# Kernel tuning notes

Hardware: AMD Instinct MI355X
Metric: run time of the kernel (lower is better)

Reference implementation:

```python
import jax, jax.numpy as jnp
import numpy as np

N = 500          # max_neurons, all alive
INPUT_SIZE = 3072
FEAT_DIM = 64
OUT_SIZE = 10
BATCH = 8192
RADIUS = 20.0
VOL = 100.0      # cubic volume (100,100,100)
N_ITER = 3


def setup_inputs() -> dict:
    key = jax.random.key(0)
    k_x, k_pos, k_iw, k_f, k_ow = jax.random.split(key, 5)
    x = jax.random.normal(k_x, (BATCH, INPUT_SIZE), dtype=jnp.float32)
    # seed positions spread across the volume, roughly matching _init_seeds
    positions = jax.random.uniform(k_pos, (N, 3), dtype=jnp.float32) * 80.0 + 10.0
    input_weights = jax.random.normal(k_iw, (N, INPUT_SIZE), dtype=jnp.float32) * 0.02
    features = jax.random.normal(k_f, (N, FEAT_DIM), dtype=jnp.float32) * 0.1
    output_weights = jax.random.normal(k_ow, (N, OUT_SIZE), dtype=jnp.float32) * 0.02
    biases = jnp.zeros((N,), dtype=jnp.float32)
    return {"x": x, "positions": positions, "input_weights": input_weights,
            "features": features, "output_weights": output_weights, "biases": biases}


def reference(x, positions, input_weights, features, output_weights, biases):
    # clamp positions into the volume (per-axis, vol is cubic here)
    pos = jnp.clip(positions, 0.1, VOL - 0.1)  # [N,3]

    # pairwise distances (grad-safe sqrt at the zero diagonal)
    diff = pos[:, None, :] - pos[None, :, :]          # [N,N,3]
    sq = jnp.sum(diff * diff, axis=-1)                # [N,N]
    pos_mask = sq > 0.0
    dist = jnp.where(pos_mask, jnp.sqrt(jnp.where(pos_mask, sq, 1.0)), 0.0)

    conn_mask = (dist < RADIUS) & (dist > 0.0)
    attenuation = jnp.exp(-dist / RADIUS) * conn_mask.astype(dist.dtype)

    # feature similarity (F.normalize clamps the norm from below at eps)
    feat_norm = features / jnp.maximum(
        jnp.linalg.norm(features, axis=1, keepdims=True), 1e-6)
    feat_sim = jnp.clip(feat_norm @ feat_norm.T, -1.0, 1.0)  # [N,N]

    conn_w = attenuation * (0.5 + 0.5 * feat_sim)
    conn_w = conn_w / (jnp.sum(conn_w, axis=1, keepdims=True) + 1e-6)

    # input gating: neurons near x=0 receive input
    x_norm = pos[:, 0] / VOL                          # [N]
    input_weight = jnp.exp(-2.0 * x_norm)
    input_weight = input_weight / (jnp.sum(input_weight) + 1e-6)

    activations = x @ input_weights.T * input_weight + biases  # [B,N]

    # iterative message passing (fixed small iteration count)
    for _ in range(N_ITER):
        msg = activations @ conn_w.T                  # [B,N]
        activations = jnp.minimum(jax.nn.relu(activations + 0.5 * msg), 50.0)

    # output gating: neurons near x=VOL emit output
    output_weight = jnp.exp(2.0 * (x_norm - 1.0))
    output_weight = output_weight / (jnp.sum(output_weight) + 1e-6)

    return activations @ (output_weights * output_weight[:, None])  # [B,OUT]
```

## Files before the change

### kernel.cpp

```cpp
#include <hip/hip_runtime.h>
#include <stdint.h>

#define N_REAL 500
#define NPAD   512
#define K_IN   3072
#define NBATCH 8192
#define NOUT   10
#define RADIUS 20.0f
#define VOLF   100.0f

typedef __attribute__((ext_vector_type(8))) __bf16 bf16x8;
typedef __attribute__((ext_vector_type(4))) float  f32x4;
typedef __attribute__((ext_vector_type(4))) unsigned short us4;

__device__ __forceinline__ unsigned short f2bf(float f) {
    unsigned int u = __float_as_uint(f);
    u += 0x7FFFu + ((u >> 16) & 1u);
    return (unsigned short)(u >> 16);
}
__device__ __forceinline__ float bf2f(unsigned short h) {
    return __uint_as_float(((unsigned int)h) << 16);
}

#define GLOBAL_AS __attribute__((address_space(1)))
#define LDS_AS    __attribute__((address_space(3)))
__device__ __forceinline__ void glds16(const void* g, void* l) {
    __builtin_amdgcn_global_load_lds((const GLOBAL_AS void*)g, (LDS_AS void*)l, 16, 0, 0);
}

__global__ void prep1(const float* __restrict__ positions,
                      const float* __restrict__ features,
                      const float* __restrict__ out_w,
                      const float* __restrict__ biases,
                      float* __restrict__ feat_norm,
                      float* __restrict__ pos_c,
                      float* __restrict__ inw,
                      float* __restrict__ biasp,
                      float* __restrict__ wout)
{
    int n = threadIdx.x;
    float e_in = 0.f, e_out = 0.f;
    float px = 0.f, py = 0.f, pz = 0.f;
    if (n < N_REAL) {
        px = fminf(fmaxf(positions[n*3+0], 0.1f), VOLF - 0.1f);
        py = fminf(fmaxf(positions[n*3+1], 0.1f), VOLF - 0.1f);
        pz = fminf(fmaxf(positions[n*3+2], 0.1f), VOLF - 0.1f);
        float xn = px / VOLF;
        e_in  = expf(-2.f * xn);
        e_out = expf(2.f * (xn - 1.f));
        float ss = 0.f;
        for (int f = 0; f < 64; ++f) { float v = features[n*64+f]; ss += v*v; }
        float nm = fmaxf(sqrtf(ss), 1e-6f);
        for (int f = 0; f < 64; ++f) feat_norm[n*64+f] = features[n*64+f] / nm;
    } else {
        for (int f = 0; f < 64; ++f) feat_norm[n*64+f] = 0.f;
    }
    pos_c[n*4+0] = px; pos_c[n*4+1] = py; pos_c[n*4+2] = pz; pos_c[n*4+3] = 0.f;

    __shared__ float s_in[512], s_out[512];
    s_in[n] = e_in; s_out[n] = e_out;
    __syncthreads();
    for (int s = 256; s > 0; s >>= 1) {
        if (n < s) { s_in[n] += s_in[n+s]; s_out[n] += s_out[n+s]; }
        __syncthreads();
    }
    float sum_in  = s_in[0]  + 1e-6f;
    float sum_out = s_out[0] + 1e-6f;

    inw[n]   = (n < N_REAL) ? (e_in / sum_in) : 0.f;
    biasp[n] = (n < N_REAL) ? biases[n] : 0.f;
    float wo = (n < N_REAL) ? (e_out / sum_out) : 0.f;
    for (int o = 0; o < NOUT; ++o)
        wout[n*NOUT + o] = (n < N_REAL) ? out_w[n*NOUT + o] * wo : 0.f;
}

__global__ void prep2(const float* __restrict__ pos_c,
                      const float* __restrict__ feat_norm,
                      unsigned short* __restrict__ conn_w)
{
    int i = blockIdx.x;
    int t = threadIdx.x;
    __shared__ float fi[64];
    __shared__ float spos[4];
    __shared__ float red[128];
    if (t < 64) fi[t] = feat_norm[i*64 + t];
    if (t < 4)  spos[t] = pos_c[i*4 + t];
    __syncthreads();

    float w[4];
    float part = 0.f;
    for (int jj = 0; jj < 4; ++jj) {
        int j = t + jj*128;
        float val = 0.f;
        if (i < N_REAL && j < N_REAL) {
            float dx = spos[0] - pos_c[j*4+0];
            float dy = spos[1] - pos_c[j*4+1];
            float dz = spos[2] - pos_c[j*4+2];
            float sq = dx*dx + dy*dy + dz*dz;
            if (sq > 0.f) {
                float dist = sqrtf(sq);
                if (dist < RADIUS) {
                    float att = expf(-dist / RADIUS);
                    float sim = 0.f;
                    const float4* fj = (const float4*)(feat_norm + j*64);
                    const float4* fi4 = (const float4*)fi;
                    #pragma unroll
                    for (int f = 0; f < 16; ++f) {
                        float4 a = fi4[f]; float4 b = fj[f];
                        sim += a.x*b.x + a.y*b.y + a.z*b.z + a.w*b.w;
                    }
                    sim = fminf(fmaxf(sim, -1.f), 1.f);
                    val = att * (0.5f + 0.5f*sim);
                }
            }
        }
        w[jj] = val; part += val;
    }
    red[t] = part;
    __syncthreads();
    for (int s = 64; s > 0; s >>= 1) {
        if (t < s) red[t] += red[t+s];
        __syncthreads();
    }
    float inv = 1.f / (red[0] + 1e-6f);
    for (int jj = 0; jj < 4; ++jj)
        conn_w[(long)i*NPAD + t + jj*128] = f2bf(w[jj] * inv);
}

__global__ void cast_pad(const float* __restrict__ src, unsigned short* __restrict__ dst,
                         long total_q, long src_q)
{
    long i = (long)blockIdx.x * blockDim.x + threadIdx.x;
    long stride = (long)gridDim.x * blockDim.x;
    for (; i < total_q; i += stride) {
        us4 o;
        if (i < src_q) {
            float4 v = ((const float4*)src)[i];
            o[0] = f2bf(v.x); o[1] = f2bf(v.y); o[2] = f2bf(v.z); o[3] = f2bf(v.w);
        } else {
            o[0] = 0; o[1] = 0; o[2] = 0; o[3] = 0;
        }
        ((us4*)dst)[i] = o;
    }
}

__device__ __forceinline__ void block_map(int b, int& m0, int& n0) {
    int xcd = b & 7, loc = b >> 3;
    m0 = (xcd*8 + (loc >> 3)) * 128;
    n0 = (loc & 7) * 64;
}

__global__ __launch_bounds__(256)
void gemm1(const float* __restrict__ X,
           const unsigned short* __restrict__ B,
           unsigned short* __restrict__ Cbf,
           const float* __restrict__ inw,
           const float* __restrict__ biasp)
{
    __shared__ unsigned short As[128*64];
    __shared__ unsigned short Bs[64*64];

    const int tid  = threadIdx.x;
    const int lane = tid & 63;
    const int wave = tid >> 6;
    int m0, n0; block_map(blockIdx.x, m0, n0);
    const int wm = (wave >> 1) * 64;
    const int wn = (wave & 1) * 32;

    f32x4 acc[4][2];
    #pragma unroll
    for (int i = 0; i < 4; ++i)
        #pragma unroll
        for (int j = 0; j < 2; ++j)
            acc[i][j] = (f32x4){0.f,0.f,0.f,0.f};

    const float4* gA[8]; unsigned short* lA[8];
    #pragma unroll
    for (int s = 0; s < 8; ++s) {
        int f = tid + s*256;
        int row = f >> 4, c4 = f & 15;
        gA[s] = (const float4*)(X + (long)(m0 + row) * K_IN) + c4;
        lA[s] = (unsigned short*)((char*)As + row*128 + ((c4*8) ^ ((row & 7) << 4)));
    }
    const char* gB[2]; char* lB[2];
    #pragma unroll
    for (int s = 0; s < 2; ++s) {
        int o = tid*16 + s*4096;
        int row = o >> 7, d = o & 127;
        gB[s] = (const char*)B + (long)(n0 + row) * (K_IN*2) + (d ^ ((row & 7) << 4));
        lB[s] = (char*)Bs + o;
    }

    for (int k0 = 0; k0 < K_IN; k0 += 64) {
        __syncthreads();
        glds16(gB[0], lB[0]);
        glds16(gB[1], lB[1]);
        gB[0] += 128; gB[1] += 128;
        float4 v[8];
        #pragma unroll
        for (int s = 0; s < 8; ++s) v[s] = gA[s][0];
        #pragma unroll
        for (int s = 0; s < 8; ++s) {
            us4 o;
            o[0] = f2bf(v[s].x); o[1] = f2bf(v[s].y);
            o[2] = f2bf(v[s].z); o[3] = f2bf(v[s].w);
            *(us4*)lA[s] = o;
            gA[s] += 16;
        }
        asm volatile("s_waitcnt vmcnt(0) lgkmcnt(0)" ::: "memory");
        __syncthreads();

        #pragma unroll
        for (int kk = 0; kk < 2; ++kk) {
            const int cb = kk*64 + (lane >> 4) * 16;
            bf16x8 af[4], bfv[2];
            #pragma unroll
            for (int i = 0; i < 4; ++i) {
                int r = wm + i*16 + (lane & 15);
                af[i] = *(const bf16x8*)((const char*)As + r*128 + (cb ^ ((r & 7) << 4)));
            }
            #pragma unroll
            for (int j = 0; j < 2; ++j) {
                int r = wn + j*16 + (lane & 15);
                bfv[j] = *(const bf16x8*)((const char*)Bs + r*128 + (cb ^ ((r & 7) << 4)));
            }
            #pragma unroll
            for (int i = 0; i < 4; ++i)
                #pragma unroll
                for (int j = 0; j < 2; ++j)
                    acc[i][j] = __builtin_amdgcn_mfma_f32_16x16x32_bf16(af[i], bfv[j], acc[i][j], 0, 0, 0);
        }
    }

    const int mbase = m0 + wm + (lane >> 4) * 4;
    const int nbase = n0 + wn + (lane & 15);
    #pragma unroll
    for (int j = 0; j < 2; ++j) {
        const int n = nbase + j*16;
        const float win = inw[n], bia = biasp[n];
        #pragma unroll
        for (int i = 0; i < 4; ++i)
            #pragma unroll
            for (int r = 0; r < 4; ++r) {
                const long m = mbase + i*16 + r;
                Cbf[m*NPAD + n] = f2bf(acc[i][j][r] * win + bia);
            }
    }
}

__global__ __launch_bounds__(256)
void gemm2(const unsigned short* __restrict__ A,
           const unsigned short* __restrict__ B,
           unsigned short* __restrict__ Cbf,
           const unsigned short* __restrict__ actOld)
{
    __shared__ unsigned short As[128*64];
    __shared__ unsigned short Bs[64*64];

    const int tid  = threadIdx.x;
    const int lane = tid & 63;
    const int wave = tid >> 6;
    int m0, n0; block_map(blockIdx.x, m0, n0);
    const int wm = (wave >> 1) * 64;
    const int wn = (wave & 1) * 32;

    f32x4 acc[4][2];
    #pragma unroll
    for (int i = 0; i < 4; ++i)
        #pragma unroll
        for (int j = 0; j < 2; ++j)
            acc[i][j] = (f32x4){0.f,0.f,0.f,0.f};

    const char* gA[4]; char* lA[4];
    #pragma unroll
    for (int s = 0; s < 4; ++s) {
        int o = tid*16 + s*4096;
        int row = o >> 7, d = o & 127;
        gA[s] = (const char*)A + (long)(m0 + row) * (NPAD*2) + (d ^ ((row & 7) << 4));
        lA[s] = (char*)As + o;
    }
    const char* gB[2]; char* lB[2];
    #pragma unroll
    for (int s = 0; s < 2; ++s) {
        int o = tid*16 + s*4096;
        int row = o >> 7, d = o & 127;
        gB[s] = (const char*)B + (long)(n0 + row) * (NPAD*2) + (d ^ ((row & 7) << 4));
        lB[s] = (char*)Bs + o;
    }

    for (int k0 = 0; k0 < NPAD; k0 += 64) {
        __syncthreads();
        #pragma unroll
        for (int s = 0; s < 4; ++s) { glds16(gA[s], lA[s]); gA[s] += 128; }
        #pragma unroll
        for (int s = 0; s < 2; ++s) { glds16(gB[s], lB[s]); gB[s] += 128; }
        asm volatile("s_waitcnt vmcnt(0)" ::: "memory");
        __syncthreads();

        #pragma unroll
        for (int kk = 0; kk < 2; ++kk) {
            const int cb = kk*64 + (lane >> 4) * 16;
            bf16x8 af[4], bfv[2];
            #pragma unroll
            for (int i = 0; i < 4; ++i) {
                int r = wm + i*16 + (lane & 15);
                af[i] = *(const bf16x8*)((const char*)As + r*128 + (cb ^ ((r & 7) << 4)));
            }
            #pragma unroll
            for (int j = 0; j < 2; ++j) {
                int r = wn + j*16 + (lane & 15);
                bfv[j] = *(const bf16x8*)((const char*)Bs + r*128 + (cb ^ ((r & 7) << 4)));
            }
            #pragma unroll
            for (int i = 0; i < 4; ++i)
                #pragma unroll
                for (int j = 0; j < 2; ++j)
                    acc[i][j] = __builtin_amdgcn_mfma_f32_16x16x32_bf16(af[i], bfv[j], acc[i][j], 0, 0, 0);
        }
    }

    const int mbase = m0 + wm + (lane >> 4) * 4;
    const int nbase = n0 + wn + (lane & 15);
    #pragma unroll
    for (int j = 0; j < 2; ++j) {
        const int n = nbase + j*16;
        #pragma unroll
        for (int i = 0; i < 4; ++i)
            #pragma unroll
            for (int r = 0; r < 4; ++r) {
                const long m = mbase + i*16 + r;
                float old = bf2f(actOld[m*NPAD + n]);
                float vv = fminf(fmaxf(old + 0.5f * acc[i][j][r], 0.f), 50.f);
                Cbf[m*NPAD + n] = f2bf(vv);
            }
    }
}

__global__ __launch_bounds__(256)
void out_gemm(const unsigned short* __restrict__ act,
              const float* __restrict__ wout,
              float* __restrict__ out)
{
    __shared__ float sw[NPAD * NOUT];
    const int tid = threadIdx.x;
    for (int i = tid; i < NPAD*NOUT; i += 256) sw[i] = wout[i];
    __syncthreads();

    const int lane = tid & 63;
    const int wv   = tid >> 6;
    const int row  = blockIdx.x * 4 + wv;

    const unsigned short* ap = act + (long)row * NPAD + lane * 8;
    us4 v0 = *(const us4*)(ap);
    us4 v1 = *(const us4*)(ap + 4);

    float p[NOUT];
    #pragma unroll
    for (int o = 0; o < NOUT; ++o) p[o] = 0.f;

    const int nb = lane * 8;
    #pragma unroll
    for (int e = 0; e < 8; ++e) {
        float a = bf2f(e < 4 ? v0[e] : v1[e-4]);
        const float* wr = &sw[(nb + e) * NOUT];
        #pragma unroll
        for (int o = 0; o < NOUT; ++o) p[o] += a * wr[o];
    }
    #pragma unroll
    for (int o = 0; o < NOUT; ++o) {
        float s = p[o];
        for (int d = 32; d > 0; d >>= 1) s += __shfl_down(s, d);
        if (lane == 0) out[(long)row * NOUT + o] = s;
    }
}

extern "C" void kernel_launch(void* const* d_in, const int* in_sizes, int n_in,
                              void* d_out, int out_size, void* d_ws, size_t ws_size,
                              hipStream_t stream)
{
    const float* x        = (const float*)d_in[0];
    const float* pos      = (const float*)d_in[1];
    const float* in_w     = (const float*)d_in[2];
    const float* feats    = (const float*)d_in[3];
    const float* out_w    = (const float*)d_in[4];
    const float* biases   = (const float*)d_in[5];
    float* out = (float*)d_out;

    char* ws = (char*)d_ws;
    unsigned short* iw_bf  = (unsigned short*)(ws);
    unsigned short* connw  = (unsigned short*)(ws + 3145728);
    unsigned short* act_a  = (unsigned short*)(ws + 3670016);
    unsigned short* act_b  = (unsigned short*)(ws + 12058624);
    float* feat_norm = (float*)(ws + 20447232);
    float* pos_c     = (float*)(ws + 20578304);
    float* inw       = (float*)(ws + 20586496);
    float* biasp     = (float*)(ws + 20588544);
    float* wout      = (float*)(ws + 20590592);

    prep1<<<1, 512, 0, stream>>>(pos, feats, out_w, biases, feat_norm, pos_c, inw, biasp, wout);
    prep2<<<512, 128, 0, stream>>>(pos_c, feat_norm, connw);
    cast_pad<<<512, 256, 0, stream>>>(in_w, iw_bf, 393216L, 384000L);

    gemm1<<<512, 256, 0, stream>>>(x, iw_bf, act_a, inw, biasp);
    gemm2<<<512, 256, 0, stream>>>(act_a, connw, act_b, act_a);
    gemm2<<<512, 256, 0, stream>>>(act_b, connw, act_a, act_b);
    gemm2<<<512, 256, 0, stream>>>(act_a, connw, act_b, act_a);

    out_gemm<<<NBATCH/4, 256, 0, stream>>>(act_b, wout, out);
}
```

Measured before the change: 133.4 us.

## Double-buffer LDS tiles in both GEMMs and prefetch the next K-step

Both GEMM kernels now hold two LDS buffers for the A and B tiles. Each iteration issues the loads for the next K-tile before running the MFMAs on the current one, so there is one barrier per iteration instead of a load-wait-compute sequence. gemm1 also switches its fp32-to-bf16 conversion to the packed v_cvt_pk_bf16_f32 instruction. gemm2 loads the old activation values before its main loop so that read overlaps the compute. This doubles LDS use and raises register pressure, which can lower occupancy.

```diff
diff --git a/kernel.cpp b/kernel.cpp
--- a/kernel.cpp
+++ b/kernel.cpp
@@ -20,6 +20,12 @@
 }
 __device__ __forceinline__ float bf2f(unsigned short h) {
     return __uint_as_float(((unsigned int)h) << 16);
+}
+__device__ __forceinline__ uint2 cvt_pk4(float4 v) {
+    uint2 r;
+    asm("v_cvt_pk_bf16_f32 %0, %1, %2" : "=v"(r.x) : "v"(v.x), "v"(v.y));
+    asm("v_cvt_pk_bf16_f32 %0, %1, %2" : "=v"(r.y) : "v"(v.z), "v"(v.w));
+    return r;
 }
 
 #define GLOBAL_AS __attribute__((address_space(1)))
@@ -157,8 +163,8 @@
            const float* __restrict__ inw,
            const float* __restrict__ biasp)
 {
-    __shared__ unsigned short As[128*64];
-    __shared__ unsigned short Bs[64*64];
+    __shared__ unsigned short As[2][128*64];
+    __shared__ unsigned short Bs[2][64*64];
 
     const int tid  = threadIdx.x;
     const int lane = tid & 63;
@@ -174,62 +180,70 @@
         for (int j = 0; j < 2; ++j)
             acc[i][j] = (f32x4){0.f,0.f,0.f,0.f};
 
-    const float4* gA[8]; unsigned short* lA[8];
+    const float4* gA[8]; int lAo[8];
     #pragma unroll
     for (int s = 0; s < 8; ++s) {
         int f = tid + s*256;
         int row = f >> 4, c4 = f & 15;
         gA[s] = (const float4*)(X + (long)(m0 + row) * K_IN) + c4;
-        lA[s] = (unsigned short*)((char*)As + row*128 + ((c4*8) ^ ((row & 7) << 4)));
-    }
-    const char* gB[2]; char* lB[2];
+        lAo[s] = row*128 + ((c4*8) ^ ((row & 7) << 4));
+    }
+    const char* gB[2]; int lBo[2];
     #pragma unroll
     for (int s = 0; s < 2; ++s) {
         int o = tid*16 + s*4096;
         int row = o >> 7, d = o & 127;
         gB[s] = (const char*)B + (long)(n0 + row) * (K_IN*2) + (d ^ ((row & 7) << 4));
-        lB[s] = (char*)Bs + o;
-    }
-
-    for (int k0 = 0; k0 < K_IN; k0 += 64) {
-        __syncthreads();
-        glds16(gB[0], lB[0]);
-        glds16(gB[1], lB[1]);
-        gB[0] += 128; gB[1] += 128;
-        float4 v[8];
-        #pragma unroll
-        for (int s = 0; s < 8; ++s) v[s] = gA[s][0];
-        #pragma unroll
-        for (int s = 0; s < 8; ++s) {
-            us4 o;
-            o[0] = f2bf(v[s].x); o[1] = f2bf(v[s].y);
-            o[2] = f2bf(v[s].z); o[3] = f2bf(v[s].w);
-            *(us4*)lA[s] = o;
-            gA[s] += 16;
-        }
-        asm volatile("s_waitcnt vmcnt(0) lgkmcnt(0)" ::: "memory");
-        __syncthreads();
-
+        lBo[s] = o;
+    }
+
+    glds16(gB[0], (char*)Bs[0] + lBo[0]);
+    glds16(gB[1], (char*)Bs[0] + lBo[1]);
+    gB[0] += 128; gB[1] += 128;
+    float4 v[8];
+    #pragma unroll
+    for (int s = 0; s < 8; ++s) { v[s] = gA[s][0]; gA[s] += 16; }
+    #pragma unroll
+    for (int s = 0; s < 8; ++s)
+        *(uint2*)((char*)As[0] + lAo[s]) = cvt_pk4(v[s]);
+    __syncthreads();
+
+    for (int t = 0; t < 48; ++t) {
+        const int cur = t & 1, nxt = cur ^ 1;
+        const bool more = (t < 47);
+        if (more) {
+            glds16(gB[0], (char*)Bs[nxt] + lBo[0]);
+            glds16(gB[1], (char*)Bs[nxt] + lBo[1]);
+            gB[0] += 128; gB[1] += 128;
+            #pragma unroll
+            for (int s = 0; s < 8; ++s) { v[s] = gA[s][0]; gA[s] += 16; }
+        }
         #pragma unroll
         for (int kk = 0; kk < 2; ++kk) {
             const int cb = kk*64 + (lane >> 4) * 16;
-            bf16x8 af[4], bfv[2];
+            bf16x8 afr[4], bfr[2];
             #pragma unroll
             for (int i = 0; i < 4; ++i) {
                 int r = wm + i*16 + (lane & 15);
-                af[i] = *(const bf16x8*)((const char*)As + r*128 + (cb ^ ((r & 7) << 4)));
+                afr[i] = *(const bf16x8*)((const char*)As[cur] + r*128 + (cb ^ ((r & 7) << 4)));
             }
             #pragma unroll
             for (int j = 0; j < 2; ++j) {
                 int r = wn + j*16 + (lane & 15);
-                bfv[j] = *(const bf16x8*)((const char*)Bs + r*128 + (cb ^ ((r & 7) << 4)));
+                bfr[j] = *(const bf16x8*)((const char*)Bs[cur] + r*128 + (cb ^ ((r & 7) << 4)));
             }
             #pragma unroll
             for (int i = 0; i < 4; ++i)
                 #pragma unroll
                 for (int j = 0; j < 2; ++j)
-                    acc[i][j] = __builtin_amdgcn_mfma_f32_16x16x32_bf16(af[i], bfv[j], acc[i][j], 0, 0, 0);
-        }
+                    acc[i][j] = __builtin_amdgcn_mfma_f32_16x16x32_bf16(afr[i], bfr[j], acc[i][j], 0, 0, 0);
+        }
+        if (more) {
+            #pragma unroll
+            for (int s = 0; s < 8; ++s)
+                *(uint2*)((char*)As[nxt] + lAo[s]) = cvt_pk4(v[s]);
+        }
+        __syncthreads();
     }
 
     const int mbase = m0 + wm + (lane >> 4) * 4;
@@ -254,8 +268,8 @@
            unsigned short* __restrict__ Cbf,
            const unsigned short* __restrict__ actOld)
 {
-    __shared__ unsigned short As[128*64];
-    __shared__ unsigned short Bs[64*64];
+    __shared__ unsigned short As[2][128*64];
+    __shared__ unsigned short Bs[2][64*64];
 
     const int tid  = threadIdx.x;
     const int lane = tid & 63;
@@ -271,56 +285,72 @@
         for (int j = 0; j < 2; ++j)
             acc[i][j] = (f32x4){0.f,0.f,0.f,0.f};
 
-    const char* gA[4]; char* lA[4];
+    const char* gA[4]; int lAo[4];
     #pragma unroll
     for (int s = 0; s < 4; ++s) {
         int o = tid*16 + s*4096;
         int row = o >> 7, d = o & 127;
         gA[s] = (const char*)A + (long)(m0 + row) * (NPAD*2) + (d ^ ((row & 7) << 4));
-        lA[s] = (char*)As + o;
-    }
-    const char* gB[2]; char* lB[2];
+        lAo[s] = o;
+    }
+    const char* gB[2]; int lBo[2];
     #pragma unroll
     for (int s = 0; s < 2; ++s) {
         int o = tid*16 + s*4096;
         int row = o >> 7, d = o & 127;
         gB[s] = (const char*)B + (long)(n0 + row) * (NPAD*2) + (d ^ ((row & 7) << 4));
-        lB[s] = (char*)Bs + o;
-    }
-
-    for (int k0 = 0; k0 < NPAD; k0 += 64) {
-        __syncthreads();
-        #pragma unroll
-        for (int s = 0; s < 4; ++s) { glds16(gA[s], lA[s]); gA[s] += 128; }
-        #pragma unroll
-        for (int s = 0; s < 2; ++s) { glds16(gB[s], lB[s]); gB[s] += 128; }
-        asm volatile("s_waitcnt vmcnt(0)" ::: "memory");
-        __syncthreads();
-
+        lBo[s] = o;
+    }
+
+    #pragma unroll
+    for (int s = 0; s < 4; ++s) { glds16(gA[s], (char*)As[0] + lAo[s]); gA[s] += 128; }
+    #pragma unroll
+    for (int s = 0; s < 2; ++s) { glds16(gB[s], (char*)Bs[0] + lBo[s]); gB[s] += 128; }
+
+    const int mbase = m0 + wm + (lane >> 4) * 4;
+    const int nbase = n0 + wn + (lane & 15);
+    unsigned short oldv[2][16];
+    #pragma unroll
+    for (int j = 0; j < 2; ++j)
+        #pragma unroll
+        for (int i = 0; i < 4; ++i)
+            #pragma unroll
+            for (int r = 0; r < 4; ++r)
+                oldv[j][i*4+r] = actOld[(long)(mbase + i*16 + r)*NPAD + nbase + j*16];
+    __syncthreads();
+
+    for (int t = 0; t < 8; ++t) {
+        const int cur = t & 1, nxt = cur ^ 1;
+        const bool more = (t < 7);
+        if (more) {
+            #pragma unroll
+            for (int s = 0; s < 4; ++s) { glds16(gA[s], (char*)As[nxt] + lAo[s]); gA[s] += 128; }
+            #pragma unroll
+            for (int s = 0; s < 2; ++s) { glds16(gB[s], (char*)Bs[nxt] + lBo[s]); gB[s] += 128; }
+        }
         #pragma unroll
         for (int kk = 0; kk < 2; ++kk) {
             const int cb = kk*64 + (lane >> 4) * 16;
-            bf16x8 af[4], bfv[2];
+            bf16x8 afr[4], bfr[2];
             #pragma unroll
             for (int i = 0; i < 4; ++i) {
                 int r = wm + i*16 + (lane & 15);
-                af[i] = *(const bf16x8*)((const char*)As + r*128 + (cb ^ ((r & 7) << 4)));
+                afr[i] = *(const bf16x8*)((const char*)As[cur] + r*128 + (cb ^ ((r & 7) << 4)));
             }
             #pragma unroll
             for (int j = 0; j < 2; ++j) {
                 int r = wn + j*16 + (lane & 15);
-                bfv[j] = *(const bf16x8*)((const char*)Bs + r*128 + (cb ^ ((r & 7) << 4)));
+                bfr[j] = *(const bf16x8*)((const char*)Bs[cur] + r*128 + (cb ^ ((r & 7) << 4)));
             }
             #pragma unroll
             for (int i = 0; i < 4; ++i)
                 #pragma unroll
                 for (int j = 0; j < 2; ++j)
-                    acc[i][j] = __builtin_amdgcn_mfma_f32_16x16x32_bf16(af[i], bfv[j], acc[i][j], 0, 0, 0);
-        }
-    }
-
-    const int mbase = m0 + wm + (lane >> 4) * 4;
-    const int nbase = n0 + wn + (lane & 15);
+                    acc[i][j] = __builtin_amdgcn_mfma_f32_16x16x32_bf16(afr[i], bfr[j], acc[i][j], 0, 0, 0);
+        }
+        __syncthreads();
+    }
+
     #pragma unroll
     for (int j = 0; j < 2; ++j) {
         const int n = nbase + j*16;
@@ -329,7 +359,7 @@
             #pragma unroll
             for (int r = 0; r < 4; ++r) {
                 const long m = mbase + i*16 + r;
-                float old = bf2f(actOld[m*NPAD + n]);
+                float old = bf2f(oldv[j][i*4+r]);
                 float vv = fminf(fmaxf(old + 0.5f * acc[i][j][r], 0.f), 50.f);
                 Cbf[m*NPAD + n] = f2bf(vv);
             }
```

Measured after the change: 130.7 us. -2.0%, faster.

## Halve GEMM M-tile to 64 rows, doubling grid to 1024 blocks

Applied to the files above, without the earlier changes.

Cuts the M tile of gemm1 and gemm2 from 128 to 64 rows and launches 1024 blocks instead of 512, so there are more blocks than the 256 CUs and load balance and occupancy improve. gemm1 now converts fp32 to bf16 with the packed v_cvt_pk_bf16_f32 instruction instead of software rounding. gemm2 prefetches the old activations before the K loop so their latency overlaps the main loop. The trade-off is twice the B-operand traffic per output and lower MFMA reuse per loaded A fragment.

```diff
diff --git a/kernel.cpp b/kernel.cpp
--- a/kernel.cpp
+++ b/kernel.cpp
@@ -20,6 +20,12 @@
 }
 __device__ __forceinline__ float bf2f(unsigned short h) {
     return __uint_as_float(((unsigned int)h) << 16);
+}
+__device__ __forceinline__ uint2 cvt_pk4(float4 v) {
+    uint2 r;
+    asm("v_cvt_pk_bf16_f32 %0, %1, %2" : "=v"(r.x) : "v"(v.x), "v"(v.y));
+    asm("v_cvt_pk_bf16_f32 %0, %1, %2" : "=v"(r.y) : "v"(v.z), "v"(v.w));
+    return r;
 }
 
 #define GLOBAL_AS __attribute__((address_space(1)))
@@ -146,7 +152,7 @@
 
 __device__ __forceinline__ void block_map(int b, int& m0, int& n0) {
     int xcd = b & 7, loc = b >> 3;
-    m0 = (xcd*8 + (loc >> 3)) * 128;
+    m0 = (xcd*16 + (loc >> 3)) * 64;
     n0 = (loc & 7) * 64;
 }
 
@@ -157,30 +163,30 @@
            const float* __restrict__ inw,
            const float* __restrict__ biasp)
 {
-    __shared__ unsigned short As[128*64];
+    __shared__ unsigned short As[64*64];
     __shared__ unsigned short Bs[64*64];
 
     const int tid  = threadIdx.x;
     const int lane = tid & 63;
     const int wave = tid >> 6;
     int m0, n0; block_map(blockIdx.x, m0, n0);
-    const int wm = (wave >> 1) * 64;
+    const int wm = (wave >> 1) * 32;
     const int wn = (wave & 1) * 32;
 
-    f32x4 acc[4][2];
-    #pragma unroll
-    for (int i = 0; i < 4; ++i)
+    f32x4 acc[2][2];
+    #pragma unroll
+    for (int i = 0; i < 2; ++i)
         #pragma unroll
         for (int j = 0; j < 2; ++j)
             acc[i][j] = (f32x4){0.f,0.f,0.f,0.f};
 
-    const float4* gA[8]; unsigned short* lA[8];
-    #pragma unroll
-    for (int s = 0; s < 8; ++s) {
+    const float4* gA[4]; int lAo[4];
+    #pragma unroll
+    for (int s = 0; s < 4; ++s) {
         int f = tid + s*256;
         int row = f >> 4, c4 = f & 15;
         gA[s] = (const float4*)(X + (long)(m0 + row) * K_IN) + c4;
-        lA[s] = (unsigned short*)((char*)As + row*128 + ((c4*8) ^ ((row & 7) << 4)));
+        lAo[s] = row*128 + ((c4*8) ^ ((row & 7) << 4));
     }
     const char* gB[2]; char* lB[2];
     #pragma unroll
@@ -191,44 +197,39 @@
         lB[s] = (char*)Bs + o;
     }
 
-    for (int k0 = 0; k0 < K_IN; k0 += 64) {
+    for (int t = 0; t < 48; ++t) {
         __syncthreads();
         glds16(gB[0], lB[0]);
         glds16(gB[1], lB[1]);
         gB[0] += 128; gB[1] += 128;
-        float4 v[8];
-        #pragma unroll
-        for (int s = 0; s < 8; ++s) v[s] = gA[s][0];
-        #pragma unroll
-        for (int s = 0; s < 8; ++s) {
-            us4 o;
-            o[0] = f2bf(v[s].x); o[1] = f2bf(v[s].y);
-            o[2] = f2bf(v[s].z); o[3] = f2bf(v[s].w);
-            *(us4*)lA[s] = o;
-            gA[s] += 16;
-        }
+        float4 v[4];
+        #pragma unroll
+        for (int s = 0; s < 4; ++s) { v[s] = gA[s][0]; gA[s] += 16; }
+        #pragma unroll
+        for (int s = 0; s < 4; ++s)
+            *(uint2*)((char*)As + lAo[s]) = cvt_pk4(v[s]);
         asm volatile("s_waitcnt vmcnt(0) lgkmcnt(0)" ::: "memory");
         __syncthreads();
 
         #pragma unroll
         for (int kk = 0; kk < 2; ++kk) {
             const int cb = kk*64 + (lane >> 4) * 16;
-            bf16x8 af[4], bfv[2];
-            #pragma unroll
-            for (int i = 0; i < 4; ++i) {
+            bf16x8 afr[2], bfr[2];
+            #pragma unroll
+            for (int i = 0; i < 2; ++i) {
                 int r = wm + i*16 + (lane & 15);
-                af[i] = *(const bf16x8*)((const char*)As + r*128 + (cb ^ ((r & 7) << 4)));
+                afr[i] = *(const bf16x8*)((const char*)As + r*128 + (cb ^ ((r & 7) << 4)));
             }
             #pragma unroll
             for (int j = 0; j < 2; ++j) {
                 int r = wn + j*16 + (lane & 15);
-                bfv[j] = *(const bf16x8*)((const char*)Bs + r*128 + (cb ^ ((r & 7) << 4)));
-            }
-            #pragma unroll
-            for (int i = 0; i < 4; ++i)
+                bfr[j] = *(const bf16x8*)((const char*)Bs + r*128 + (cb ^ ((r & 7) << 4)));
+            }
+            #pragma unroll
+            for (int i = 0; i < 2; ++i)
                 #pragma unroll
                 for (int j = 0; j < 2; ++j)
-                    acc[i][j] = __builtin_amdgcn_mfma_f32_16x16x32_bf16(af[i], bfv[j], acc[i][j], 0, 0, 0);
+                    acc[i][j] = __builtin_amdgcn_mfma_f32_16x16x32_bf16(afr[i], bfr[j], acc[i][j], 0, 0, 0);
         }
     }
 
@@ -239,7 +240,7 @@
         const int n = nbase + j*16;
         const float win = inw[n], bia = biasp[n];
         #pragma unroll
-        for (int i = 0; i < 4; ++i)
+        for (int i = 0; i < 2; ++i)
             #pragma unroll
             for (int r = 0; r < 4; ++r) {
                 const long m = mbase + i*16 + r;
@@ -254,26 +255,26 @@
            unsigned short* __restrict__ Cbf,
            const unsigned short* __restrict__ actOld)
 {
-    __shared__ unsigned short As[128*64];
+    __shared__ unsigned short As[64*64];
     __shared__ unsigned short Bs[64*64];
 
     const int tid  = threadIdx.x;
     const int lane = tid & 63;
     const int wave = tid >> 6;
     int m0, n0; block_map(blockIdx.x, m0, n0);
-    const int wm = (wave >> 1) * 64;
+    const int wm = (wave >> 1) * 32;
     const int wn = (wave & 1) * 32;
 
-    f32x4 acc[4][2];
-    #pragma unroll
-    for (int i = 0; i < 4; ++i)
+    f32x4 acc[2][2];
+    #pragma unroll
+    for (int i = 0; i < 2; ++i)
         #pragma unroll
         for (int j = 0; j < 2; ++j)
             acc[i][j] = (f32x4){0.f,0.f,0.f,0.f};
 
-    const char* gA[4]; char* lA[4];
-    #pragma unroll
-    for (int s = 0; s < 4; ++s) {
+    const char* gA[2]; char* lA[2];
+    #pragma unroll
+    for (int s = 0; s < 2; ++s) {
         int o = tid*16 + s*4096;
         int row = o >> 7, d = o & 127;
         gA[s] = (const char*)A + (long)(m0 + row) * (NPAD*2) + (d ^ ((row & 7) << 4));
@@ -288,10 +289,21 @@
         lB[s] = (char*)Bs + o;
     }
 
-    for (int k0 = 0; k0 < NPAD; k0 += 64) {
-        __syncthreads();
-        #pragma unroll
-        for (int s = 0; s < 4; ++s) { glds16(gA[s], lA[s]); gA[s] += 128; }
+    const int mbase = m0 + wm + (lane >> 4) * 4;
+    const int nbase = n0 + wn + (lane & 15);
+    unsigned short oldv[2][8];
+    #pragma unroll
+    for (int j = 0; j < 2; ++j)
+        #pragma unroll
+        for (int i = 0; i < 2; ++i)
+            #pragma unroll
+            for (int r = 0; r < 4; ++r)
+                oldv[j][i*4+r] = actOld[(long)(mbase + i*16 + r)*NPAD + nbase + j*16];
+
+    for (int t = 0; t < 8; ++t) {
+        __syncthreads();
+        #pragma unroll
+        for (int s = 0; s < 2; ++s) { glds16(gA[s], lA[s]); gA[s] += 128; }
         #pragma unroll
         for (int s = 0; s < 2; ++s) { glds16(gB[s], lB[s]); gB[s] += 128; }
         asm volatile("s_waitcnt vmcnt(0)" ::: "memory");
@@ -300,36 +312,34 @@
         #pragma unroll
         for (int kk = 0; kk < 2; ++kk) {
             const int cb = kk*64 + (lane >> 4) * 16;
-            bf16x8 af[4], bfv[2];
-            #pragma unroll
-            for (int i = 0; i < 4; ++i) {
+            bf16x8 afr[2], bfr[2];
+            #pragma unroll
+            for (int i = 0; i < 2; ++i) {
                 int r = wm + i*16 + (lane & 15);
-                af[i] = *(const bf16x8*)((const char*)As + r*128 + (cb ^ ((r & 7) << 4)));
+                afr[i] = *(const bf16x8*)((const char*)As + r*128 + (cb ^ ((r & 7) << 4)));
             }
             #pragma unroll
             for (int j = 0; j < 2; ++j) {
                 int r = wn + j*16 + (lane & 15);
-                bfv[j] = *(const bf16x8*)((const char*)Bs + r*128 + (cb ^ ((r & 7) << 4)));
-            }
-            #pragma unroll
-            for (int i = 0; i < 4; ++i)
+                bfr[j] = *(const bf16x8*)((const char*)Bs + r*128 + (cb ^ ((r & 7) << 4)));
+            }
+            #pragma unroll
+            for (int i = 0; i < 2; ++i)
                 #pragma unroll
                 for (int j = 0; j < 2; ++j)
-                    acc[i][j] = __builtin_amdgcn_mfma_f32_16x16x32_bf16(af[i], bfv[j], acc[i][j], 0, 0, 0);
+                    acc[i][j] = __builtin_amdgcn_mfma_f32_16x16x32_bf16(afr[i], bfr[j], acc[i][j], 0, 0, 0);
         }
     }
 
-    const int mbase = m0 + wm + (lane >> 4) * 4;
-    const int nbase = n0 + wn + (lane & 15);
     #pragma unroll
     for (int j = 0; j < 2; ++j) {
         const int n = nbase + j*16;
         #pragma unroll
-        for (int i = 0; i < 4; ++i)
+        for (int i = 0; i < 2; ++i)
             #pragma unroll
             for (int r = 0; r < 4; ++r) {
                 const long m = mbase + i*16 + r;
-                float old = bf2f(actOld[m*NPAD + n]);
+                float old = bf2f(oldv[j][i*4+r]);
                 float vv = fminf(fmaxf(old + 0.5f * acc[i][j][r], 0.f), 50.f);
                 Cbf[m*NPAD + n] = f2bf(vv);
             }
@@ -401,10 +411,10 @@
     prep2<<<512, 128, 0, stream>>>(pos_c, feat_norm, connw);
     cast_pad<<<512, 256, 0, stream>>>(in_w, iw_bf, 393216L, 384000L);
 
-    gemm1<<<512, 256, 0, stream>>>(x, iw_bf, act_a, inw, biasp);
-    gemm2<<<512, 256, 0, stream>>>(act_a, connw, act_b, act_a);
-    gemm2<<<512, 256, 0, stream>>>(act_b, connw, act_a, act_b);
-    gemm2<<<512, 256, 0, stream>>>(act_a, connw, act_b, act_a);
+    gemm1<<<1024, 256, 0, stream>>>(x, iw_bf, act_a, inw, biasp);
+    gemm2<<<1024, 256, 0, stream>>>(act_a, connw, act_b, act_a);
+    gemm2<<<1024, 256, 0, stream>>>(act_b, connw, act_a, act_b);
+    gemm2<<<1024, 256, 0, stream>>>(act_a, connw, act_b, act_a);
 
     out_gemm<<<NBATCH/4, 256, 0, stream>>>(act_b, wout, out);
 }
```

Result: faster. 127.2 us (-4.6%).
